# Performance work log

Hardware: AMD Instinct MI355X
Metric: run time of the kernel (lower is better)

The kernel has to match this reference:

```python
import jax, jax.numpy as jnp
import numpy as np

NUM_POINTS = 32
POINT_DIM = 4
HIDDEN_DIM = 256
BATCH = 8192


def setup_inputs() -> dict:
    key = jax.random.key(0)
    k1, k2, k3 = jax.random.split(key, 3)
    path_data = jax.random.normal(k1, (BATCH, NUM_POINTS * POINT_DIM), dtype=jnp.float32)
    # per-step Linear(point_dim+hidden_dim -> hidden_dim); torch Linear weight layout [out, in]
    fan_in = POINT_DIM + HIDDEN_DIM
    scale = 1.0 / np.sqrt(fan_in)
    W = jax.random.uniform(k2, (NUM_POINTS, HIDDEN_DIM, fan_in), dtype=jnp.float32, minval=-scale, maxval=scale)
    b = jax.random.uniform(k3, (NUM_POINTS, HIDDEN_DIM), dtype=jnp.float32, minval=-scale, maxval=scale)
    return {"path_data": path_data, "W": W, "b": b}


def reference(path_data, W, b):
    P, H = W.shape[0], W.shape[1]
    B = path_data.shape[0]
    pd = W.shape[2] - H
    # chunks: [P, B, point_dim]
    chunks = path_data.reshape(B, P, pd).transpose(1, 0, 2)

    def step(h, xs):
        wp, Wi, bi = xs
        # concat order matches torch: (curr_hidden, current_wp)
        combined = jnp.concatenate([h, wp], axis=1)  # [B, H+pd]
        h_new = jax.nn.relu(combined @ Wi.T + bi)    # [B, H]
        return h_new, h_new

    h0 = jnp.zeros((B, H), dtype=path_data.dtype)
    _, feats = jax.lax.scan(step, h0, (chunks, W, b))  # feats: [P, B, H]
    return feats.transpose(1, 0, 2).reshape(B, P * H)
```

## Files before the change

### kernel.cpp

```cpp
#include <hip/hip_runtime.h>

typedef __attribute__((ext_vector_type(8))) short bf16x8;
typedef __attribute__((ext_vector_type(16))) float f32x16;
typedef __attribute__((ext_vector_type(4))) float f32x4;

#define NPTS 32
#define HID 256
#define FANIN 260
#define NKB 17
#define OUTSTRIDE 8192

__device__ __forceinline__ unsigned short f2bf(float f) {
  unsigned u = __builtin_bit_cast(unsigned, f);
  u += 0x7fffu + ((u >> 16) & 1u);
  return (unsigned short)(u >> 16);
}

__global__ __launch_bounds__(256) void prep_kernel(
    const float* __restrict__ W, const float* __restrict__ bias,
    bf16x8* __restrict__ pack) {
  __shared__ float wl[32 * FANIN];
  const int p = blockIdx.x >> 3;
  const int nb = blockIdx.x & 7;
  const int t = threadIdx.x;
  const f32x4* src = reinterpret_cast<const f32x4*>(
      W + ((size_t)p * HID + nb * 32) * FANIN);
  for (int i = t; i < 32 * FANIN / 4; i += 256)
    *reinterpret_cast<f32x4*>(wl + i * 4) = src[i];
  __syncthreads();
  const int lane = t & 63;
  const int wv = t >> 6;
  const int m = lane & 31;
  const int g = lane >> 5;
  const float* rowp = wl + m * FANIN;
  for (int kb = wv; kb < NKB; kb += 4) {
    unsigned short e[8];
#pragma unroll
    for (int i = 0; i < 8; ++i) e[i] = 0;
    if (kb < 16) {
      int k0 = kb * 16 + g * 8;
#pragma unroll
      for (int i = 0; i < 8; ++i) e[i] = f2bf(rowp[k0 + i]);
    } else if (g == 0) {
      e[0] = f2bf(rowp[256]);
      e[1] = f2bf(rowp[257]);
      e[2] = f2bf(rowp[258]);
      e[3] = f2bf(rowp[259]);
      e[4] = f2bf(bias[p * HID + nb * 32 + m]);
    }
    bf16x8 v;
#pragma unroll
    for (int i = 0; i < 8; ++i) v[i] = (short)e[i];
    pack[(((size_t)p * 8 + nb) * NKB + kb) * 64 + lane] = v;
  }
}

__global__ __launch_bounds__(512, 2) void enc_kernel(
    const float* __restrict__ path, const bf16x8* __restrict__ pack,
    float* __restrict__ out) {
  __shared__ __align__(16) char lds[32768];
  const int tid = threadIdx.x;
  const int lane = tid & 63;
  const int w = tid >> 6;
  const int col = lane & 31;
  const int g = lane >> 5;
  const int b0 = blockIdx.x * 32;
  const int swz = col << 4;

  {
    f32x4 z = {0.0f, 0.0f, 0.0f, 0.0f};
    *reinterpret_cast<f32x4*>(lds + tid * 32) = z;
    *reinterpret_cast<f32x4*>(lds + tid * 32 + 16) = z;
  }

  const float4* prow =
      reinterpret_cast<const float4*>(path + (size_t)(b0 + col) * 128);
  float* outbase = out + (size_t)b0 * OUTSTRIDE + w * 32 + col;

  bf16x8 BC[NKB];
  {
    const bf16x8* Bp0 = pack + (size_t)w * NKB * 64 + lane;
#pragma unroll
    for (int kb = 0; kb < NKB; ++kb) BC[kb] = Bp0[kb * 64];
  }
  float4 px = prow[0];
  __syncthreads();

  for (int p = 0; p < NPTS; ++p) {
    const int pn = (p + 1 < NPTS) ? p + 1 : 0;
    const bf16x8* Bnp = pack + ((size_t)(pn * 8 + w) * NKB) * 64 + lane;
    const char* hb = lds + (p & 1) * 16384;

    bf16x8 a[16];
#pragma unroll
    for (int kb = 0; kb < 16; ++kb)
      a[kb] = *reinterpret_cast<const bf16x8*>(
          hb + col * 512 + ((kb * 32 + g * 16) ^ swz));

    bf16x8 ax;
#pragma unroll
    for (int i = 0; i < 8; ++i) ax[i] = 0;
    if (g == 0) {
      ax[0] = (short)f2bf(px.x);
      ax[1] = (short)f2bf(px.y);
      ax[2] = (short)f2bf(px.z);
      ax[3] = (short)f2bf(px.w);
      ax[4] = (short)0x3F80;
    }

    f32x16 acc0, acc1;
#pragma unroll
    for (int i = 0; i < 16; ++i) {
      acc0[i] = 0.0f;
      acc1[i] = 0.0f;
    }

    __builtin_amdgcn_s_setprio(1);
#pragma unroll
    for (int kb = 0; kb < 16; ++kb) {
      if (kb & 1)
        acc1 = __builtin_amdgcn_mfma_f32_32x32x16_bf16(a[kb], BC[kb], acc1, 0, 0, 0);
      else
        acc0 = __builtin_amdgcn_mfma_f32_32x32x16_bf16(a[kb], BC[kb], acc0, 0, 0, 0);
      BC[kb] = Bnp[kb * 64];
    }
    acc0 = __builtin_amdgcn_mfma_f32_32x32x16_bf16(ax, BC[16], acc0, 0, 0, 0);
    __builtin_amdgcn_s_setprio(0);
    BC[16] = Bnp[16 * 64];
    px = prow[pn];

    char* hn = lds + ((p + 1) & 1) * 16384;
    float vr[16];
#pragma unroll
    for (int r = 0; r < 16; ++r) {
      int rr = (r & 3) + 8 * (r >> 2) + 4 * g;
      float v = fmaxf(acc0[r] + acc1[r], 0.0f);
      vr[r] = v;
      *reinterpret_cast<unsigned short*>(
          hn + rr * 512 + (((w * 32 + col) * 2) ^ (rr << 4))) = f2bf(v);
    }
    float* outp = outbase + p * 256;
#pragma unroll
    for (int r = 0; r < 16; ++r) {
      int rr = (r & 3) + 8 * (r >> 2) + 4 * g;
      __builtin_nontemporal_store(vr[r], outp + (size_t)rr * OUTSTRIDE);
    }
    asm volatile("s_waitcnt lgkmcnt(0)" ::: "memory");
    __builtin_amdgcn_s_barrier();
  }
}

extern "C" void kernel_launch(void* const* d_in, const int* in_sizes, int n_in,
                              void* d_out, int out_size, void* d_ws,
                              size_t ws_size, hipStream_t stream) {
  const float* path = (const float*)d_in[0];
  const float* W = (const float*)d_in[1];
  const float* bias = (const float*)d_in[2];
  float* out = (float*)d_out;
  bf16x8* pack = (bf16x8*)d_ws;

  prep_kernel<<<256, 256, 0, stream>>>(W, bias, pack);
  enc_kernel<<<256, 512, 0, stream>>>(path, pack, out);
}
```

Before: 115.0 us.

## Split K across two wave halves with LDS reduction of partial sums

Doubles the block to 1024 threads. Each output column tile is now computed by two waves, each covering half of the K dimension (one of them also handles the input and bias block). The partial accumulators are exchanged through a swizzled LDS staging area and then reduced. Each wave finishes half of the rows for the ReLU, the output store and the next hidden-state write. This is meant to shorten the serial MFMA chain per recurrent step and to cut per-wave register pressure, at the cost of an extra LDS round trip and an extra barrier each step.

```diff
diff --git a/kernel.cpp b/kernel.cpp
--- a/kernel.cpp
+++ b/kernel.cpp
@@ -55,95 +55,102 @@
   }
 }
 
-__global__ __launch_bounds__(512, 2) void enc_kernel(
+__global__ __launch_bounds__(1024, 4) void enc_kernel(
     const float* __restrict__ path, const bf16x8* __restrict__ pack,
     float* __restrict__ out) {
-  __shared__ __align__(16) char lds[32768];
+  __shared__ __align__(16) char lds[65536];
   const int tid = threadIdx.x;
   const int lane = tid & 63;
-  const int w = tid >> 6;
+  const int wv = tid >> 6;
+  const int t = wv & 7;
+  const int half = wv >> 3;
   const int col = lane & 31;
   const int g = lane >> 5;
   const int b0 = blockIdx.x * 32;
   const int swz = col << 4;
+  const int sswz = (col & 7) << 4;
 
   {
     f32x4 z = {0.0f, 0.0f, 0.0f, 0.0f};
-    *reinterpret_cast<f32x4*>(lds + tid * 32) = z;
-    *reinterpret_cast<f32x4*>(lds + tid * 32 + 16) = z;
+    *reinterpret_cast<f32x4*>(lds + tid * 16) = z;
   }
 
   const float4* prow =
       reinterpret_cast<const float4*>(path + (size_t)(b0 + col) * 128);
-  float* outbase = out + (size_t)b0 * OUTSTRIDE + w * 32 + col;
+  float* outbase = out + (size_t)b0 * OUTSTRIDE + t * 32 + col;
 
-  bf16x8 BC[NKB];
+  bf16x8 BC[9];
   {
-    const bf16x8* Bp0 = pack + (size_t)w * NKB * 64 + lane;
+    const bf16x8* Bp0 = pack + ((size_t)t * NKB + half * 8) * 64 + lane;
 #pragma unroll
-    for (int kb = 0; kb < NKB; ++kb) BC[kb] = Bp0[kb * 64];
+    for (int i = 0; i < 8; ++i) BC[i] = Bp0[i * 64];
+    if (half) BC[8] = *(pack + ((size_t)t * NKB + 16) * 64 + lane);
   }
   float4 px = prow[0];
   __syncthreads();
 
   for (int p = 0; p < NPTS; ++p) {
     const int pn = (p + 1 < NPTS) ? p + 1 : 0;
-    const bf16x8* Bnp = pack + ((size_t)(pn * 8 + w) * NKB) * 64 + lane;
+    const bf16x8* Bnp =
+        pack + (((size_t)(pn * 8 + t)) * NKB + half * 8) * 64 + lane;
     const char* hb = lds + (p & 1) * 16384;
 
-    bf16x8 a[16];
+    f32x16 acc;
 #pragma unroll
-    for (int kb = 0; kb < 16; ++kb)
-      a[kb] = *reinterpret_cast<const bf16x8*>(
-          hb + col * 512 + ((kb * 32 + g * 16) ^ swz));
+    for (int i = 0; i < 16; ++i) acc[i] = 0.0f;
 
-    bf16x8 ax;
 #pragma unroll
-    for (int i = 0; i < 8; ++i) ax[i] = 0;
-    if (g == 0) {
-      ax[0] = (short)f2bf(px.x);
-      ax[1] = (short)f2bf(px.y);
-      ax[2] = (short)f2bf(px.z);
-      ax[3] = (short)f2bf(px.w);
-      ax[4] = (short)0x3F80;
+    for (int i = 0; i < 8; ++i) {
+      const int kbg = half * 8 + i;
+      bf16x8 a = *reinterpret_cast<const bf16x8*>(
+          hb + col * 512 + ((kbg * 32 + g * 16) ^ swz));
+      acc = __builtin_amdgcn_mfma_f32_32x32x16_bf16(a, BC[i], acc, 0, 0, 0);
+      BC[i] = Bnp[i * 64];
     }
-
-    f32x16 acc0, acc1;
+    if (half) {
+      bf16x8 ax;
 #pragma unroll
-    for (int i = 0; i < 16; ++i) {
-      acc0[i] = 0.0f;
-      acc1[i] = 0.0f;
+      for (int i = 0; i < 8; ++i) ax[i] = 0;
+      if (g == 0) {
+        ax[0] = (short)f2bf(px.x);
+        ax[1] = (short)f2bf(px.y);
+        ax[2] = (short)f2bf(px.z);
+        ax[3] = (short)f2bf(px.w);
+        ax[4] = (short)0x3F80;
+      }
+      acc = __builtin_amdgcn_mfma_f32_32x32x16_bf16(ax, BC[8], acc, 0, 0, 0);
+      BC[8] = *(pack + (((size_t)(pn * 8 + t)) * NKB + 16) * 64 + lane);
     }
-
-    __builtin_amdgcn_s_setprio(1);
-#pragma unroll
-    for (int kb = 0; kb < 16; ++kb) {
-      if (kb & 1)
-        acc1 = __builtin_amdgcn_mfma_f32_32x32x16_bf16(a[kb], BC[kb], acc1, 0, 0, 0);
-      else
-        acc0 = __builtin_amdgcn_mfma_f32_32x32x16_bf16(a[kb], BC[kb], acc0, 0, 0, 0);
-      BC[kb] = Bnp[kb * 64];
-    }
-    acc0 = __builtin_amdgcn_mfma_f32_32x32x16_bf16(ax, BC[16], acc0, 0, 0, 0);
-    __builtin_amdgcn_s_setprio(0);
-    BC[16] = Bnp[16 * 64];
     px = prow[pn];
 
+    char* stg = lds + 32768 + t * 4096 + col * 128;
+    const int wrow = (half ^ 1) * 16 + 4 * g;
+    {
+      const int wr = (half ^ 1) * 8;
+      f32x4 v0 = {acc[wr], acc[wr + 1], acc[wr + 2], acc[wr + 3]};
+      f32x4 v1 = {acc[wr + 4], acc[wr + 5], acc[wr + 6], acc[wr + 7]};
+      *reinterpret_cast<f32x4*>(stg + ((wrow * 4) ^ sswz)) = v0;
+      *reinterpret_cast<f32x4*>(stg + (((wrow + 8) * 4) ^ sswz)) = v1;
+    }
+    asm volatile("s_waitcnt lgkmcnt(0)" ::: "memory");
+    __builtin_amdgcn_s_barrier();
+
+    const int rrow = half * 16 + 4 * g;
+    f32x4 u0 = *reinterpret_cast<const f32x4*>(stg + ((rrow * 4) ^ sswz));
+    f32x4 u1 =
+        *reinterpret_cast<const f32x4*>(stg + (((rrow + 8) * 4) ^ sswz));
+
     char* hn = lds + ((p + 1) & 1) * 16384;
-    float vr[16];
+    float* outp = outbase + p * 256;
+    const int kr = half * 8;
 #pragma unroll
-    for (int r = 0; r < 16; ++r) {
-      int rr = (r & 3) + 8 * (r >> 2) + 4 * g;
-      float v = fmaxf(acc0[r] + acc1[r], 0.0f);
-      vr[r] = v;
+    for (int j = 0; j < 8; ++j) {
+      const int rr = half * 16 + (j & 3) + 8 * (j >> 2) + 4 * g;
+      float part = (j < 4) ? u0[j & 3] : u1[j & 3];
+      float v = fmaxf(acc[kr + j] + part, 0.0f);
+      __builtin_nontemporal_store(v, outp + (size_t)rr * OUTSTRIDE);
       *reinterpret_cast<unsigned short*>(
-          hn + rr * 512 + (((w * 32 + col) * 2) ^ (rr << 4))) = f2bf(v);
-    }
-    float* outp = outbase + p * 256;
-#pragma unroll
-    for (int r = 0; r < 16; ++r) {
-      int rr = (r & 3) + 8 * (r >> 2) + 4 * g;
-      __builtin_nontemporal_store(vr[r], outp + (size_t)rr * OUTSTRIDE);
+          hn + rr * 512 + (((t * 32 + col) * 2) ^ (rr << 4))) = f2bf(v);
     }
     asm volatile("s_waitcnt lgkmcnt(0)" ::: "memory");
     __builtin_amdgcn_s_barrier();
@@ -160,5 +167,5 @@
   bf16x8* pack = (bf16x8*)d_ws;
 
   prep_kernel<<<256, 256, 0, stream>>>(W, bias, pack);
-  enc_kernel<<<256, 512, 0, stream>>>(path, pack, out);
+  enc_kernel<<<256, 1024, 0, stream>>>(path, pack, out);
 }
```

Measured after the change: 176.9 us. 53.8% more time.

## Process 64 batch rows per block to reuse register-resident weights across two M tiles

Applied to the files above, without the earlier changes.

Each block now handles 64 batch rows instead of 32, with each wave running two 32x32 MFMA tiles that share the same B fragment. This doubles the reuse of the weight registers loaded per step and halves the weight traffic from global memory per row. The cost is half as many blocks (128 on a chip with 256 CUs), a doubled LDS footprint, and the removal of the split-K dual accumulators and the setprio hints. The A-fragment loads are now interleaved with the MFMAs rather than preloaded.

```diff
diff --git a/kernel.cpp b/kernel.cpp
--- a/kernel.cpp
+++ b/kernel.cpp
@@ -58,23 +58,26 @@
 __global__ __launch_bounds__(512, 2) void enc_kernel(
     const float* __restrict__ path, const bf16x8* __restrict__ pack,
     float* __restrict__ out) {
-  __shared__ __align__(16) char lds[32768];
+  __shared__ __align__(16) char lds[65536];
   const int tid = threadIdx.x;
   const int lane = tid & 63;
   const int w = tid >> 6;
   const int col = lane & 31;
   const int g = lane >> 5;
-  const int b0 = blockIdx.x * 32;
+  const int b0 = blockIdx.x * 64;
   const int swz = col << 4;
 
   {
     f32x4 z = {0.0f, 0.0f, 0.0f, 0.0f};
-    *reinterpret_cast<f32x4*>(lds + tid * 32) = z;
-    *reinterpret_cast<f32x4*>(lds + tid * 32 + 16) = z;
+#pragma unroll
+    for (int s = 0; s < 4; ++s)
+      *reinterpret_cast<f32x4*>(lds + tid * 64 + s * 16) = z;
   }
 
-  const float4* prow =
+  const float4* prow0 =
       reinterpret_cast<const float4*>(path + (size_t)(b0 + col) * 128);
+  const float4* prow1 =
+      reinterpret_cast<const float4*>(path + (size_t)(b0 + 32 + col) * 128);
   float* outbase = out + (size_t)b0 * OUTSTRIDE + w * 32 + col;
 
   bf16x8 BC[NKB];
@@ -83,30 +86,14 @@
 #pragma unroll
     for (int kb = 0; kb < NKB; ++kb) BC[kb] = Bp0[kb * 64];
   }
-  float4 px = prow[0];
+  float4 px0 = prow0[0];
+  float4 px1 = prow1[0];
   __syncthreads();
 
   for (int p = 0; p < NPTS; ++p) {
     const int pn = (p + 1 < NPTS) ? p + 1 : 0;
     const bf16x8* Bnp = pack + ((size_t)(pn * 8 + w) * NKB) * 64 + lane;
-    const char* hb = lds + (p & 1) * 16384;
-
-    bf16x8 a[16];
-#pragma unroll
-    for (int kb = 0; kb < 16; ++kb)
-      a[kb] = *reinterpret_cast<const bf16x8*>(
-          hb + col * 512 + ((kb * 32 + g * 16) ^ swz));
-
-    bf16x8 ax;
-#pragma unroll
-    for (int i = 0; i < 8; ++i) ax[i] = 0;
-    if (g == 0) {
-      ax[0] = (short)f2bf(px.x);
-      ax[1] = (short)f2bf(px.y);
-      ax[2] = (short)f2bf(px.z);
-      ax[3] = (short)f2bf(px.w);
-      ax[4] = (short)0x3F80;
-    }
+    const char* hb = lds + (p & 1) * 32768;
 
     f32x16 acc0, acc1;
 #pragma unroll
@@ -115,35 +102,55 @@
       acc1[i] = 0.0f;
     }
 
-    __builtin_amdgcn_s_setprio(1);
 #pragma unroll
     for (int kb = 0; kb < 16; ++kb) {
-      if (kb & 1)
-        acc1 = __builtin_amdgcn_mfma_f32_32x32x16_bf16(a[kb], BC[kb], acc1, 0, 0, 0);
-      else
-        acc0 = __builtin_amdgcn_mfma_f32_32x32x16_bf16(a[kb], BC[kb], acc0, 0, 0, 0);
+      const int off = (kb * 32 + g * 16) ^ swz;
+      bf16x8 a0 = *reinterpret_cast<const bf16x8*>(hb + col * 512 + off);
+      bf16x8 a1 =
+          *reinterpret_cast<const bf16x8*>(hb + (col + 32) * 512 + off);
+      acc0 = __builtin_amdgcn_mfma_f32_32x32x16_bf16(a0, BC[kb], acc0, 0, 0, 0);
+      acc1 = __builtin_amdgcn_mfma_f32_32x32x16_bf16(a1, BC[kb], acc1, 0, 0, 0);
       BC[kb] = Bnp[kb * 64];
     }
-    acc0 = __builtin_amdgcn_mfma_f32_32x32x16_bf16(ax, BC[16], acc0, 0, 0, 0);
-    __builtin_amdgcn_s_setprio(0);
-    BC[16] = Bnp[16 * 64];
-    px = prow[pn];
+    {
+      bf16x8 ax0, ax1;
+#pragma unroll
+      for (int i = 0; i < 8; ++i) {
+        ax0[i] = 0;
+        ax1[i] = 0;
+      }
+      if (g == 0) {
+        ax0[0] = (short)f2bf(px0.x);
+        ax0[1] = (short)f2bf(px0.y);
+        ax0[2] = (short)f2bf(px0.z);
+        ax0[3] = (short)f2bf(px0.w);
+        ax0[4] = (short)0x3F80;
+        ax1[0] = (short)f2bf(px1.x);
+        ax1[1] = (short)f2bf(px1.y);
+        ax1[2] = (short)f2bf(px1.z);
+        ax1[3] = (short)f2bf(px1.w);
+        ax1[4] = (short)0x3F80;
+      }
+      acc0 = __builtin_amdgcn_mfma_f32_32x32x16_bf16(ax0, BC[16], acc0, 0, 0, 0);
+      acc1 = __builtin_amdgcn_mfma_f32_32x32x16_bf16(ax1, BC[16], acc1, 0, 0, 0);
+      BC[16] = Bnp[16 * 64];
+    }
+    px0 = prow0[pn];
+    px1 = prow1[pn];
 
-    char* hn = lds + ((p + 1) & 1) * 16384;
-    float vr[16];
-#pragma unroll
-    for (int r = 0; r < 16; ++r) {
-      int rr = (r & 3) + 8 * (r >> 2) + 4 * g;
-      float v = fmaxf(acc0[r] + acc1[r], 0.0f);
-      vr[r] = v;
-      *reinterpret_cast<unsigned short*>(
-          hn + rr * 512 + (((w * 32 + col) * 2) ^ (rr << 4))) = f2bf(v);
-    }
+    char* hn = lds + ((p + 1) & 1) * 32768;
     float* outp = outbase + p * 256;
 #pragma unroll
-    for (int r = 0; r < 16; ++r) {
-      int rr = (r & 3) + 8 * (r >> 2) + 4 * g;
-      __builtin_nontemporal_store(vr[r], outp + (size_t)rr * OUTSTRIDE);
+    for (int ms = 0; ms < 2; ++ms) {
+#pragma unroll
+      for (int r = 0; r < 16; ++r) {
+        const int rr = (r & 3) + 8 * (r >> 2) + 4 * g;
+        const int row = ms * 32 + rr;
+        float v = fmaxf((ms ? acc1[r] : acc0[r]), 0.0f);
+        *reinterpret_cast<unsigned short*>(
+            hn + row * 512 + (((w * 32 + col) * 2) ^ (rr << 4))) = f2bf(v);
+        __builtin_nontemporal_store(v, outp + (size_t)row * OUTSTRIDE);
+      }
     }
     asm volatile("s_waitcnt lgkmcnt(0)" ::: "memory");
     __builtin_amdgcn_s_barrier();
@@ -160,5 +167,5 @@
   bf16x8* pack = (bf16x8*)d_ws;
 
   prep_kernel<<<256, 256, 0, stream>>>(W, bias, pack);
-  enc_kernel<<<256, 512, 0, stream>>>(path, pack, out);
+  enc_kernel<<<128, 512, 0, stream>>>(path, pack, out);
 }
```

Result: slower. 130.9 us (+13.8%).
